# Optimization experiments

Measured on AMD Instinct MI355X. Metric: run time of the kernel, lower is better.

Reference implementation:

```python
import jax, jax.numpy as jnp
import numpy as np

B, S, E = 2, 4096, 1024
H = 16
W = 256  # attention_window == chunk size; attn width = 3*W


def _chunk3(x):
    # x: [b, nc, w, h, d] -> stack (prev, cur, next) chunks on last axis: [b, nc, w, h, d, 3]
    prev = jnp.pad(x[:, :-1], ((0, 0), (1, 0), (0, 0), (0, 0), (0, 0)))
    nxt = jnp.pad(x[:, 1:], ((0, 0), (0, 1), (0, 0), (0, 0), (0, 0)))
    return jnp.stack([prev, x, nxt], axis=-1)


def setup_inputs() -> dict:
    key = jax.random.key(0)
    ks = jax.random.split(key, 4)
    hs = jax.random.normal(ks[0], (B, S, E), jnp.float32)

    def lin(k):
        kw, kb = jax.random.split(k)
        return (jax.random.normal(kw, (E, E), jnp.float32) * 0.02,
                jax.random.normal(kb, (E,), jnp.float32) * 0.02)

    Wq, bq = lin(ks[1])
    Wk, bk = lin(ks[2])
    Wv, bv = lin(ks[3])
    return {"hidden_states": hs, "Wq": Wq, "bq": bq, "Wk": Wk, "bk": bk, "Wv": Wv, "bv": bv}


def reference(hidden_states, Wq, bq, Wk, bk, Wv, bv):
    b, s, e = hidden_states.shape
    h, w = H, W
    d = e // h
    nc = s // w  # number of non-overlapping chunks

    # torch nn.Linear: y = x @ W.T + b ; q scaled by 1/sqrt(head_dim)
    q = (hidden_states @ Wq.T + bq) * (1.0 / np.sqrt(d))
    k = hidden_states @ Wk.T + bk
    v = hidden_states @ Wv.T + bv
    q = q.reshape(b, s, h, d)
    k = k.reshape(b, s, h, d)
    v = v.reshape(b, s, h, d)

    # ---- sliding_chunks_no_overlap_matmul_qk ----
    cq = q.reshape(b, nc, w, h, d)
    ck3 = _chunk3(k.reshape(b, nc, w, h, d))  # [b,nc,w,h,d,3]
    # [b,nc,w,h,3,w] -> [b,s,h,3w]
    scores = jnp.einsum('bcxhd,bcyhde->bcxhey', cq, ck3).reshape(b, s, h, 3 * w)

    # ---- mask_invalid_locations (same math as Longformer's helper) ----
    ii = jnp.arange(w)[:, None]
    cc = jnp.arange(w + 1)[None, :]
    beg_mask = cc < (w - ii)   # [w, w+1] applied to first w rows, first w+1 cols
    end_mask = cc >= (w - ii)  # flipped mask, last w rows, last w+1 cols
    neg_inf = jnp.array(-jnp.inf, scores.dtype)
    beg = jnp.where(beg_mask[None, :, None, :], neg_inf, scores[:, :w, :, :w + 1])
    scores = scores.at[:, :w, :, :w + 1].set(beg)
    end = jnp.where(end_mask[None, :, None, :], neg_inf, scores[:, s - w:, :, 3 * w - (w + 1):])
    scores = scores.at[:, s - w:, :, 3 * w - (w + 1):].set(end)

    # softmax in float32 (as in original), cast back
    probs = jax.nn.softmax(scores.astype(jnp.float32), axis=-1).astype(hidden_states.dtype)

    # ---- sliding_chunks_no_overlap_matmul_pv ----
    cp = probs.reshape(b, nc, w, h, 3, w)          # bcwhpd (d = key pos in chunk)
    cv3 = _chunk3(v.reshape(b, nc, w, h, d))       # bcdhep (d = pos, e = head_dim, p = 3)
    attn = jnp.einsum('bcwhpd,bcdhep->bcwhe', cp, cv3).reshape(b, s, h, d)

    return attn.reshape(b, s, e)
```

## Files before the change

kernel.cpp:

```cpp
#include <hip/hip_runtime.h>
#include <math.h>

#define BB  2
#define SS  4096
#define EE  1024
#define HH  16
#define DD  64
#define WW  256
#define NCC 16
#define MTOT (BB*SS)

typedef __attribute__((ext_vector_type(4))) float f32x4;
typedef __attribute__((ext_vector_type(8))) short bf16x8;

__device__ __forceinline__ void gl_lds16(const void* g, void* l) {
  __builtin_amdgcn_global_load_lds(
      (const __attribute__((address_space(1))) unsigned int*)g,
      (__attribute__((address_space(3))) unsigned int*)l,
      16, 0, 0);
}

__device__ __forceinline__ unsigned bf16rne(float f) {
  unsigned u = __float_as_uint(f);
  return (u + (((u >> 16) & 1u) + 0x7fffu)) >> 16;
}

__device__ __forceinline__ unsigned long long pack64(unsigned a, unsigned b,
                                                     unsigned c2, unsigned d) {
  return (unsigned long long)(a | (b << 16)) |
         ((unsigned long long)(c2 | (d << 16)) << 32);
}

__global__ __launch_bounds__(256) void split_all(
    const float* __restrict__ hs, const float* __restrict__ Wq,
    const float* __restrict__ Wk, const float* __restrict__ Wv,
    unsigned short* __restrict__ Ahi, unsigned short* __restrict__ Alo,
    unsigned short* __restrict__ Wqh, unsigned short* __restrict__ Wql,
    unsigned short* __restrict__ Wkh, unsigned short* __restrict__ Wkl,
    unsigned short* __restrict__ Wvh, unsigned short* __restrict__ Wvl)
{
  const int bx = blockIdx.x;
  const float* src; unsigned short *hi, *lo; size_t blk;
  if (bx < 8192)       { src = hs; hi = Ahi; lo = Alo; blk = bx; }
  else if (bx < 9216)  { src = Wq; hi = Wqh; lo = Wql; blk = bx - 8192; }
  else if (bx < 10240) { src = Wk; hi = Wkh; lo = Wkl; blk = bx - 9216; }
  else                 { src = Wv; hi = Wvh; lo = Wvl; blk = bx - 10240; }

  const size_t i = blk * 256 + threadIdx.x;
  const float4 v = ((const float4*)src)[i];
  float f[4] = {v.x, v.y, v.z, v.w};
  unsigned short h[4], l[4];
  #pragma unroll
  for (int j = 0; j < 4; ++j) {
    unsigned u  = __float_as_uint(f[j]);
    unsigned uh = u & 0xFFFF0000u;
    h[j] = (unsigned short)(uh >> 16);
    float r = f[j] - __uint_as_float(uh);
    unsigned ur = __float_as_uint(r);
    ur += ((ur >> 16) & 1u) + 0x7FFFu;
    l[j] = (unsigned short)(ur >> 16);
  }
  *(ushort4*)&hi[4*i] = make_ushort4(h[0], h[1], h[2], h[3]);
  *(ushort4*)&lo[4*i] = make_ushort4(l[0], l[1], l[2], l[3]);
}

struct ProjArgs {
  const unsigned short* Wh;
  const unsigned short* Wl;
  const float* bias;
  unsigned short* outHi;
  unsigned short* outLo;
  float scale;
};

__global__ __launch_bounds__(256) void mfma_proj(
    const unsigned short* __restrict__ Ahi,
    const unsigned short* __restrict__ Alo,
    ProjArgs p0, ProjArgs p1, ProjArgs p2)
{
  __shared__ __align__(16) union {
    unsigned short stage[2][4][4096];
    unsigned short ep[128][136];
  } sh;

  const int tid  = threadIdx.x;
  const int lane = tid & 63;
  const int wid  = tid >> 6;
  const int wr   = wid >> 1, wc = wid & 1;
  const int m0   = blockIdx.x * 128, n0 = blockIdx.y * 128;
  const ProjArgs P = (blockIdx.z == 0) ? p0 : ((blockIdx.z == 1) ? p1 : p2);

  const int q0 = tid, q1 = 256 + tid;
  const int row0 = ((q0 >> 5) << 3) | (q0 & 7), kc0 = (q0 >> 3) & 3;
  const int row1 = ((q1 >> 5) << 3) | (q1 & 7), kc1 = (q1 >> 3) & 3;

  const size_t aoff0 = (size_t)(m0 + row0) * 2048 + (size_t)(kc0 * 16);
  const size_t aoff1 = (size_t)(m0 + row1) * 2048 + (size_t)(kc1 * 16);
  const size_t boff0 = (size_t)(n0 + row0) * 2048 + (size_t)(kc0 * 16);
  const size_t boff1 = (size_t)(n0 + row1) * 2048 + (size_t)(kc1 * 16);

  const int dst0 = (wid * 64) * 16;
  const int dst1 = (256 + wid * 64) * 16;

  const char* gAh = (const char*)Ahi;
  const char* gAl = (const char*)Alo;
  const char* gBh = (const char*)P.Wh;
  const char* gBl = (const char*)P.Wl;

  const int fr = lane & 15;
  const int kc = lane >> 4;
  int a_o[4], b_o[4];
  #pragma unroll
  for (int f = 0; f < 4; ++f) {
    int r = wr * 64 + f * 16 + fr;
    a_o[f] = ((r >> 3) << 9) | (kc << 7) | ((r & 7) << 4);
    r = wc * 64 + f * 16 + fr;
    b_o[f] = ((r >> 3) << 9) | (kc << 7) | ((r & 7) << 4);
  }

  f32x4 acc[4][4];
  #pragma unroll
  for (int i = 0; i < 4; ++i)
    #pragma unroll
    for (int j = 0; j < 4; ++j) acc[i][j] = (f32x4){0.f, 0.f, 0.f, 0.f};

  char* const Lp = (char*)&sh.stage[0][0][0];
  #define PL(b, p) (Lp + (((b)*4 + (p)) * 8192))

  #define STAGE(buf, ks) { const size_t kb = (size_t)(ks) * 64; \
    gl_lds16(gAh + aoff0 + kb, PL(buf,0) + dst0); \
    gl_lds16(gAh + aoff1 + kb, PL(buf,0) + dst1); \
    gl_lds16(gAl + aoff0 + kb, PL(buf,1) + dst0); \
    gl_lds16(gAl + aoff1 + kb, PL(buf,1) + dst1); \
    gl_lds16(gBh + boff0 + kb, PL(buf,2) + dst0); \
    gl_lds16(gBh + boff1 + kb, PL(buf,2) + dst1); \
    gl_lds16(gBl + boff0 + kb, PL(buf,3) + dst0); \
    gl_lds16(gBl + boff1 + kb, PL(buf,3) + dst1); }

  #define COMPUTE(buf) { \
    bf16x8 ah[4], al[4], bh[4], bl[4]; \
    _Pragma("unroll") \
    for (int f = 0; f < 4; ++f) { \
      ah[f] = *(const bf16x8*)(PL(buf,0) + a_o[f]); \
      al[f] = *(const bf16x8*)(PL(buf,1) + a_o[f]); \
      bh[f] = *(const bf16x8*)(PL(buf,2) + b_o[f]); \
      bl[f] = *(const bf16x8*)(PL(buf,3) + b_o[f]); \
    } \
    _Pragma("unroll") \
    for (int i = 0; i < 4; ++i) \
      _Pragma("unroll") \
      for (int j = 0; j < 4; ++j) \
        acc[i][j] = __builtin_amdgcn_mfma_f32_16x16x32_bf16(ah[i], bh[j], acc[i][j], 0,0,0); \
    _Pragma("unroll") \
    for (int i = 0; i < 4; ++i) \
      _Pragma("unroll") \
      for (int j = 0; j < 4; ++j) \
        acc[i][j] = __builtin_amdgcn_mfma_f32_16x16x32_bf16(ah[i], bl[j], acc[i][j], 0,0,0); \
    _Pragma("unroll") \
    for (int i = 0; i < 4; ++i) \
      _Pragma("unroll") \
      for (int j = 0; j < 4; ++j) \
        acc[i][j] = __builtin_amdgcn_mfma_f32_16x16x32_bf16(al[i], bh[j], acc[i][j], 0,0,0); }

  STAGE(0, 0);
  __syncthreads();
  for (int ks = 0; ks < 32; ks += 2) {
    STAGE(1, ks + 1);
    COMPUTE(0);
    __syncthreads();
    if (ks + 2 < 32) STAGE(0, ks + 2);
    COMPUTE(1);
    __syncthreads();
  }
  #undef PL
  #undef STAGE
  #undef COMPUTE

  const int r4 = (lane >> 4) << 2;

  #define EP_PASS(PLANE, OUTPTR) { \
    __syncthreads(); \
    _Pragma("unroll") \
    for (int j = 0; j < 4; ++j) { \
      const int col_l = wc*64 + j*16 + fr; \
      const float bv = P.bias[n0 + col_l]; \
      _Pragma("unroll") \
      for (int i = 0; i < 4; ++i) { \
        const int rl0 = wr*64 + i*16 + r4; \
        _Pragma("unroll") \
        for (int v = 0; v < 4; ++v) { \
          const float val = (acc[i][j][v] + bv) * P.scale; \
          const unsigned u = __float_as_uint(val); \
          unsigned sv; \
          if (PLANE == 0) { sv = u >> 16; } \
          else { \
            const float rres = val - __uint_as_float(u & 0xFFFF0000u); \
            unsigned ur = __float_as_uint(rres); \
            ur += ((ur >> 16) & 1u) + 0x7FFFu; sv = ur >> 16; \
          } \
          const int rl = rl0 + v; \
          sh.ep[rl][(((col_l >> 3) ^ (rl & 7)) << 3) + (col_l & 7)] = \
              (unsigned short)sv; \
        } \
      } \
    } \
    __syncthreads(); \
    _Pragma("unroll") \
    for (int u2 = 0; u2 < 8; ++u2) { \
      const int chunk = u2 * 256 + tid; \
      const int rr = chunk >> 4, c16 = chunk & 15; \
      const bf16x8 vv = *(const bf16x8*)&sh.ep[rr][(c16 ^ (rr & 7)) << 3]; \
      *(bf16x8*)&OUTPTR[(size_t)(m0 + rr) * EE + n0 + c16*8] = vv; \
    } }

  EP_PASS(0, P.outHi)
  EP_PASS(1, P.outLo)
  #undef EP_PASS
}

__global__ __launch_bounds__(256, 2) void attn_mfma(
    const unsigned short* __restrict__ Qh_g, const unsigned short* __restrict__ Ql_g,
    const unsigned short* __restrict__ Kh_g, const unsigned short* __restrict__ Kl_g,
    const unsigned short* __restrict__ Vh_g, const unsigned short* __restrict__ Vl_g,
    float* __restrict__ Og)
{
  __shared__ __align__(16) unsigned short Kf[2][2048];
  __shared__ __align__(16) unsigned short Vt[2][2048];
  __shared__ unsigned long long Pscr[4][256];

  const int c = blockIdx.x, h = blockIdx.y, b = blockIdx.z;
  const int tid = threadIdx.x;
  const int lane = tid & 63, wid = tid >> 6;
  const int g = lane >> 4, lq = lane & 15;

  const size_t qrow0 = (size_t)(b * NCC + c) * WW;
  const int colh = h * DD;

  bf16x8 qfh[4][2], qfl[4][2];
  #pragma unroll
  for (int s = 0; s < 4; ++s)
    #pragma unroll
    for (int ch = 0; ch < 2; ++ch) {
      const size_t off = (qrow0 + wid*64 + s*16 + lq) * EE + colh + ch*32 + g*8;
      qfh[s][ch] = *(const bf16x8*)(Qh_g + off);
      qfl[s][ch] = *(const bf16x8*)(Ql_g + off);
    }

  f32x4 Oa[4][4];
  #pragma unroll
  for (int i = 0; i < 4; ++i)
    #pragma unroll
    for (int j = 0; j < 4; ++j) Oa[i][j] = (f32x4){0.f, 0.f, 0.f, 0.f};
  float m[4], lsum[4];
  #pragma unroll
  for (int s = 0; s < 4; ++s) { m[s] = -1e30f; lsum[s] = 0.f; }

  const int kK = 16*(wid & 1) + lq;
  const int dK = 32*(wid >> 1) + g*8;
  const int stv = tid >> 5, idxv = tid & 31;
  const int kV = 16*(stv >> 2) + (idxv >> 1);
  const int dV = 16*(stv & 3) + 8*(idxv & 1);
  const int C0  = ((dV >> 4) << 6) | ((kV >> 3) << 4) | (dV & 15);
  const int swW = (((dV >> 4) & 1) << 2) | (((kV >> 3) & 1) << 1) | ((dV >> 3) & 1);
  const int vel = kV & 7;

  const long krow0_base = (long)qrow0 - WW;
  const int t0 = (c == 0) ? 8 : 0;
  const int tN = (c == NCC-1) ? 16 : 24;

  uint4 rkh, rkl, rvh, rvl;
  {
    const long kr = krow0_base + (long)t0*32;
    const size_t offK = (size_t)(kr + kK) * EE + colh + dK;
    const size_t offV = (size_t)(kr + kV) * EE + colh + dV;
    rkh = *(const uint4*)(Kh_g + offK); rkl = *(const uint4*)(Kl_g + offK);
    rvh = *(const uint4*)(Vh_g + offV); rvl = *(const uint4*)(Vl_g + offV);
  }

  for (int tt = t0; tt < tN; ++tt) {
    __syncthreads();
    *(uint4*)&Kf[0][wid*512 + lane*8] = rkh;
    *(uint4*)&Kf[1][wid*512 + lane*8] = rkl;
    {
      const unsigned hw[4] = {rvh.x, rvh.y, rvh.z, rvh.w};
      const unsigned lw[4] = {rvl.x, rvl.y, rvl.z, rvl.w};
      #pragma unroll
      for (int t = 0; t < 8; ++t) {
        const int ii = C0*8 + ((t ^ swW) << 3) + vel;
        Vt[0][ii] = (unsigned short)(hw[t >> 1] >> ((t & 1) * 16));
        Vt[1][ii] = (unsigned short)(lw[t >> 1] >> ((t & 1) * 16));
      }
    }
    __syncthreads();

    if (tt + 1 < tN) {
      const long kr = krow0_base + (long)(tt+1)*32;
      const size_t offK = (size_t)(kr + kK) * EE + colh + dK;
      const size_t offV = (size_t)(kr + kV) * EE + colh + dV;
      rkh = *(const uint4*)(Kh_g + offK); rkl = *(const uint4*)(Kl_g + offK);
      rvh = *(const uint4*)(Vh_g + offV); rvl = *(const uint4*)(Vl_g + offV);
    }

    bf16x8 kfh[2][2], kfl[2][2];
    #pragma unroll
    for (int f = 0; f < 4; ++f) {
      const int o = f*512 + lane*8;
      kfh[f & 1][f >> 1] = *(const bf16x8*)&Kf[0][o];
      kfl[f & 1][f >> 1] = *(const bf16x8*)&Kf[1][o];
    }

    bf16x8 vfh[4], vfl[4];
    #pragma unroll
    for (int ds = 0; ds < 4; ++ds) {
      const int rch = ds*64 + g*16 + lq;
      const int rsw = (((rch >> 6) & 1) << 2) | (((rch >> 4) & 1) << 1) | ((rch >> 3) & 1);
      vfh[ds] = *(const bf16x8*)&Vt[0][(rch ^ rsw) * 8];
      vfl[ds] = *(const bf16x8*)&Vt[1][(rch ^ rsw) * 8];
    }

    #pragma unroll
    for (int s = 0; s < 4; ++s) {
      f32x4 ac0 = (f32x4){0.f,0.f,0.f,0.f}, ac1 = (f32x4){0.f,0.f,0.f,0.f};
      #pragma unroll
      for (int ch = 0; ch < 2; ++ch) {
        ac0 = __builtin_amdgcn_mfma_f32_16x16x32_bf16(kfh[0][ch], qfh[s][ch], ac0, 0,0,0);
        ac0 = __builtin_amdgcn_mfma_f32_16x16x32_bf16(kfh[0][ch], qfl[s][ch], ac0, 0,0,0);
        ac0 = __builtin_amdgcn_mfma_f32_16x16x32_bf16(kfl[0][ch], qfh[s][ch], ac0, 0,0,0);
        ac1 = __builtin_amdgcn_mfma_f32_16x16x32_bf16(kfh[1][ch], qfh[s][ch], ac1, 0,0,0);
        ac1 = __builtin_amdgcn_mfma_f32_16x16x32_bf16(kfh[1][ch], qfl[s][ch], ac1, 0,0,0);
        ac1 = __builtin_amdgcn_mfma_f32_16x16x32_bf16(kfl[1][ch], qfh[s][ch], ac1, 0,0,0);
      }

      float tmax = fmaxf(fmaxf(fmaxf(ac0[0],ac0[1]), fmaxf(ac0[2],ac0[3])),
                         fmaxf(fmaxf(ac1[0],ac1[1]), fmaxf(ac1[2],ac1[3])));
      tmax = fmaxf(tmax, __shfl_xor(tmax, 16));
      tmax = fmaxf(tmax, __shfl_xor(tmax, 32));
      const float mo = m[s];
      const float mn = fmaxf(mo, tmax);
      m[s] = mn;
      const float sc = __expf(mo - mn);
      float pv[8];
      #pragma unroll
      for (int r = 0; r < 4; ++r) { pv[r] = __expf(ac0[r] - mn); pv[4+r] = __expf(ac1[r] - mn); }
      float ps = 0.f;
      #pragma unroll
      for (int r = 0; r < 8; ++r) ps += pv[r];
      lsum[s] = lsum[s] * sc + ps;
      #pragma unroll
      for (int ds = 0; ds < 4; ++ds) Oa[ds][s] *= sc;

      unsigned hb[8], lb[8];
      #pragma unroll
      for (int r = 0; r < 8; ++r) {
        hb[r] = bf16rne(pv[r]);
        const float rr = pv[r] - __uint_as_float(hb[r] << 16);
        lb[r] = bf16rne(rr);
      }
      const int pq = (g >> 1)*32 + lq*2 + (g & 1);
      Pscr[wid][pq]            = pack64(hb[0],hb[1],hb[2],hb[3]);
      Pscr[wid][pq + 64]       = pack64(hb[4],hb[5],hb[6],hb[7]);
      Pscr[wid][128 + pq]      = pack64(lb[0],lb[1],lb[2],lb[3]);
      Pscr[wid][128 + pq + 64] = pack64(lb[4],lb[5],lb[6],lb[7]);
      asm volatile("" ::: "memory");
      union U8 { unsigned long long q[2]; bf16x8 v; };
      U8 uh, ul;
      uh.q[0] = Pscr[wid][lane*2];       uh.q[1] = Pscr[wid][lane*2 + 1];
      ul.q[0] = Pscr[wid][128 + lane*2]; ul.q[1] = Pscr[wid][128 + lane*2 + 1];
      const bf16x8 pbh = uh.v;
      const bf16x8 pbl = ul.v;

      #pragma unroll
      for (int ds = 0; ds < 4; ++ds) {
        Oa[ds][s] = __builtin_amdgcn_mfma_f32_16x16x32_bf16(vfh[ds], pbh, Oa[ds][s], 0,0,0);
        Oa[ds][s] = __builtin_amdgcn_mfma_f32_16x16x32_bf16(vfl[ds], pbh, Oa[ds][s], 0,0,0);
        Oa[ds][s] = __builtin_amdgcn_mfma_f32_16x16x32_bf16(vfh[ds], pbl, Oa[ds][s], 0,0,0);
      }
    }
  }

  #pragma unroll
  for (int s = 0; s < 4; ++s) {
    float ls = lsum[s];
    ls += __shfl_xor(ls, 16);
    ls += __shfl_xor(ls, 32);
    const int x = wid*64 + s*16 + lq;
    const float nz = (c == 0) ? (float)x
                   : ((c == NCC-1) ? (float)(WW - 1 - x) : 0.f);
    ls += nz * __expf(0.f - m[s]);
    const float inv = 1.f / ls;
    float* op = Og + (qrow0 + x) * EE + colh;
    #pragma unroll
    for (int ds = 0; ds < 4; ++ds) {
      float4 r;
      r.x = Oa[ds][s][0]*inv; r.y = Oa[ds][s][1]*inv;
      r.z = Oa[ds][s][2]*inv; r.w = Oa[ds][s][3]*inv;
      *(float4*)(op + ds*16 + g*4) = r;
    }
  }
}

extern "C" void kernel_launch(void* const* d_in, const int* in_sizes, int n_in,
                              void* d_out, int out_size, void* d_ws, size_t ws_size,
                              hipStream_t stream) {
    const float* hs = (const float*)d_in[0];
    const float* Wq = (const float*)d_in[1];
    const float* bq = (const float*)d_in[2];
    const float* Wk = (const float*)d_in[3];
    const float* bk = (const float*)d_in[4];
    const float* Wv = (const float*)d_in[5];
    const float* bv = (const float*)d_in[6];
    float* out = (float*)d_out;

    const size_t mat  = (size_t)MTOT * EE;
    const size_t wmat = (size_t)EE * EE;

    unsigned short* w = (unsigned short*)d_ws;
    unsigned short* Ahi = w;            unsigned short* Alo = Ahi + mat;
    unsigned short* Wqh = Alo + mat;    unsigned short* Wql = Wqh + wmat;
    unsigned short* Wkh = Wql + wmat;   unsigned short* Wkl = Wkh + wmat;
    unsigned short* Wvh = Wkl + wmat;   unsigned short* Wvl = Wvh + wmat;
    unsigned short* Qhb = Wvl + wmat;   unsigned short* Qlb = Qhb + mat;
    unsigned short* Khb = Qlb + mat;    unsigned short* Klb = Khb + mat;
    unsigned short* Vhb = Klb + mat;    unsigned short* Vlb = Vhb + mat;

    split_all<<<8192 + 3*1024, 256, 0, stream>>>(
        hs, Wq, Wk, Wv, Ahi, Alo, Wqh, Wql, Wkh, Wkl, Wvh, Wvl);

    ProjArgs pq{Wqh, Wql, bq, Qhb, Qlb, 0.125f};
    ProjArgs pk{Wkh, Wkl, bk, Khb, Klb, 1.0f};
    ProjArgs pv{Wvh, Wvl, bv, Vhb, Vlb, 1.0f};
    dim3 g(MTOT/128, EE/128, 3);
    mfma_proj<<<g, 256, 0, stream>>>(Ahi, Alo, pq, pk, pv);

    dim3 ga(NCC, HH, BB);
    attn_mfma<<<ga, 256, 0, stream>>>(Qhb, Qlb, Khb, Klb, Vhb, Vlb, out);
}
```

Before: 342.9 us.

## Load projection weight fragments directly from global into registers, halve LDS staging

The B-operand (weight hi/lo) tiles are no longer staged through LDS. Each wave loads its bf16x8 fragments straight from global memory into double-buffered registers, and only the activation planes are staged. This halves LDS staging traffic and footprint, and launch bounds now request 2 blocks per SU. The trade-off is that every wave redundantly fetches B from global/L2 (waves sharing wc duplicate loads), register pressure rises from the extra fragment buffers, and the 2-block launch bound may force spills.

Measured after the change: 424.9 us. 23.9% more time.

```diff
diff --git a/kernel.cpp b/kernel.cpp
--- a/kernel.cpp
+++ b/kernel.cpp
@@ -73,13 +73,13 @@
   float scale;
 };
 
-__global__ __launch_bounds__(256) void mfma_proj(
+__global__ __launch_bounds__(256, 2) void mfma_proj(
     const unsigned short* __restrict__ Ahi,
     const unsigned short* __restrict__ Alo,
     ProjArgs p0, ProjArgs p1, ProjArgs p2)
 {
   __shared__ __align__(16) union {
-    unsigned short stage[2][4][4096];
+    unsigned short stage[2][2][4096];
     unsigned short ep[128][136];
   } sh;
 
@@ -96,26 +96,24 @@
 
   const size_t aoff0 = (size_t)(m0 + row0) * 2048 + (size_t)(kc0 * 16);
   const size_t aoff1 = (size_t)(m0 + row1) * 2048 + (size_t)(kc1 * 16);
-  const size_t boff0 = (size_t)(n0 + row0) * 2048 + (size_t)(kc0 * 16);
-  const size_t boff1 = (size_t)(n0 + row1) * 2048 + (size_t)(kc1 * 16);
 
   const int dst0 = (wid * 64) * 16;
   const int dst1 = (256 + wid * 64) * 16;
 
   const char* gAh = (const char*)Ahi;
   const char* gAl = (const char*)Alo;
-  const char* gBh = (const char*)P.Wh;
-  const char* gBl = (const char*)P.Wl;
+  const unsigned short* gBh16 = P.Wh;
+  const unsigned short* gBl16 = P.Wl;
 
   const int fr = lane & 15;
   const int kc = lane >> 4;
-  int a_o[4], b_o[4];
+  int a_o[4];
+  unsigned b_go[4];
   #pragma unroll
   for (int f = 0; f < 4; ++f) {
     int r = wr * 64 + f * 16 + fr;
     a_o[f] = ((r >> 3) << 9) | (kc << 7) | ((r & 7) << 4);
-    r = wc * 64 + f * 16 + fr;
-    b_o[f] = ((r >> 3) << 9) | (kc << 7) | ((r & 7) << 4);
+    b_go[f] = (unsigned)((n0 + wc * 64 + f * 16 + fr) * EE + kc * 8);
   }
 
   f32x4 acc[4][4];
@@ -125,55 +123,64 @@
     for (int j = 0; j < 4; ++j) acc[i][j] = (f32x4){0.f, 0.f, 0.f, 0.f};
 
   char* const Lp = (char*)&sh.stage[0][0][0];
-  #define PL(b, p) (Lp + (((b)*4 + (p)) * 8192))
+  #define PL(b, p) (Lp + (((b)*2 + (p)) * 8192))
 
   #define STAGE(buf, ks) { const size_t kb = (size_t)(ks) * 64; \
     gl_lds16(gAh + aoff0 + kb, PL(buf,0) + dst0); \
     gl_lds16(gAh + aoff1 + kb, PL(buf,0) + dst1); \
     gl_lds16(gAl + aoff0 + kb, PL(buf,1) + dst0); \
-    gl_lds16(gAl + aoff1 + kb, PL(buf,1) + dst1); \
-    gl_lds16(gBh + boff0 + kb, PL(buf,2) + dst0); \
-    gl_lds16(gBh + boff1 + kb, PL(buf,2) + dst1); \
-    gl_lds16(gBl + boff0 + kb, PL(buf,3) + dst0); \
-    gl_lds16(gBl + boff1 + kb, PL(buf,3) + dst1); }
-
-  #define COMPUTE(buf) { \
-    bf16x8 ah[4], al[4], bh[4], bl[4]; \
+    gl_lds16(gAl + aoff1 + kb, PL(buf,1) + dst1); }
+
+  #define LOADB(BH, BL, ks) { \
+    _Pragma("unroll") \
+    for (int f = 0; f < 4; ++f) { \
+      BH[f] = *(const bf16x8*)(gBh16 + b_go[f] + (unsigned)((ks) * 32)); \
+      BL[f] = *(const bf16x8*)(gBl16 + b_go[f] + (unsigned)((ks) * 32)); \
+    } }
+
+  #define COMPUTE(buf, BH, BL) { \
+    bf16x8 ah[4], al[4]; \
     _Pragma("unroll") \
     for (int f = 0; f < 4; ++f) { \
       ah[f] = *(const bf16x8*)(PL(buf,0) + a_o[f]); \
       al[f] = *(const bf16x8*)(PL(buf,1) + a_o[f]); \
-      bh[f] = *(const bf16x8*)(PL(buf,2) + b_o[f]); \
-      bl[f] = *(const bf16x8*)(PL(buf,3) + b_o[f]); \
     } \
     _Pragma("unroll") \
     for (int i = 0; i < 4; ++i) \
       _Pragma("unroll") \
       for (int j = 0; j < 4; ++j) \
-        acc[i][j] = __builtin_amdgcn_mfma_f32_16x16x32_bf16(ah[i], bh[j], acc[i][j], 0,0,0); \
+        acc[i][j] = __builtin_amdgcn_mfma_f32_16x16x32_bf16(ah[i], BH[j], acc[i][j], 0,0,0); \
     _Pragma("unroll") \
     for (int i = 0; i < 4; ++i) \
       _Pragma("unroll") \
       for (int j = 0; j < 4; ++j) \
-        acc[i][j] = __builtin_amdgcn_mfma_f32_16x16x32_bf16(ah[i], bl[j], acc[i][j], 0,0,0); \
+        acc[i][j] = __builtin_amdgcn_mfma_f32_16x16x32_bf16(ah[i], BL[j], acc[i][j], 0,0,0); \
     _Pragma("unroll") \
     for (int i = 0; i < 4; ++i) \
       _Pragma("unroll") \
       for (int j = 0; j < 4; ++j) \
-        acc[i][j] = __builtin_amdgcn_mfma_f32_16x16x32_bf16(al[i], bh[j], acc[i][j], 0,0,0); }
+        acc[i][j] = __builtin_amdgcn_mfma_f32_16x16x32_bf16(al[i], BH[j], acc[i][j], 0,0,0); }
+
+  bf16x8 bhA[4], blA[4], bhB[4], blB[4];
 
   STAGE(0, 0);
+  LOADB(bhA, blA, 0);
   __syncthreads();
   for (int ks = 0; ks < 32; ks += 2) {
     STAGE(1, ks + 1);
-    COMPUTE(0);
+    LOADB(bhB, blB, ks + 1);
+    COMPUTE(0, bhA, blA);
     __syncthreads();
-    if (ks + 2 < 32) STAGE(0, ks + 2);
-    COMPUTE(1);
+    if (ks + 2 < 32) {
+      STAGE(0, ks + 2);
+      LOADB(bhA, blA, ks + 2);
+    }
+    COMPUTE(1, bhB, blB);
     __syncthreads();
   }
   #undef PL
   #undef STAGE
+  #undef LOADB
   #undef COMPUTE
 
   const int r4 = (lane >> 4) << 2;
```
